# Kernel tuning notes

Measured on AMD Instinct MI355X. Metric: run time of the kernel, lower is better.

Reference implementation:

```python
import jax, jax.numpy as jnp
import numpy as np

DT = 1.0
V_LAMBDA = 1e-4
V_RIDGE = 1e-4


def third_order_D(Np):
    # [Np-3, Np] banded third-difference operator
    M = Np - 3
    r = jnp.arange(M)
    D = jnp.zeros((M, Np), dtype=jnp.float32)
    D = D.at[r, r].set(-1.0).at[r, r + 1].set(3.0).at[r, r + 2].set(-3.0).at[r, r + 3].set(1.0)
    return D


def setup_inputs() -> dict:
    key = jax.random.key(0)
    k1, k2, k3 = jax.random.split(key, 3)
    B, N = 8192, 64
    dxy = jax.random.normal(k1, (B, N, 2), dtype=jnp.float32)
    theta = jax.random.normal(k2, (B, N + 1), dtype=jnp.float32)
    v0 = jax.random.normal(k3, (B,), dtype=jnp.float32)
    return {"dxy": dxy, "theta": theta, "v0": v0}


def reference(dxy, theta, v0):
    B, N, _ = dxy.shape  # theta: [B, N+1]
    g = (2.0 / DT) * dxy                     # [B, N, 2]
    b = g.reshape(B, 2 * N)                  # interleaved (x, y) per step
    cos_t = jnp.cos(theta)
    sin_t = jnp.sin(theta)

    # Assemble banded data matrix A: [B, 2N, N+1]
    rows = jnp.arange(N)
    A = jnp.zeros((B, 2 * N, N + 1), dtype=dxy.dtype)
    A = A.at[:, 2 * rows, rows].set(cos_t[:, :-1])
    A = A.at[:, 2 * rows, rows + 1].set(cos_t[:, 1:])
    A = A.at[:, 2 * rows + 1, rows].set(sin_t[:, :-1])
    A = A.at[:, 2 * rows + 1, rows + 1].set(sin_t[:, 1:])
    # data weights w = 1 -> Aw == A

    ATA = jnp.einsum('bij,bik->bjk', A, A)           # [B, N+1, N+1]
    rhs = jnp.einsum('bij,bi->bj', A[:, :, 1:], b)   # [B, N]
    rhs = rhs - ATA[:, 1:, 0] * v0[:, None]

    # Smoothness prior: third-order difference, lam3 = v_lambda / dt^6
    D3 = third_order_D(N + 1)
    DTD = (V_LAMBDA / DT ** 6) * (D3.T @ D3)         # [N+1, N+1], shared across batch
    rhs = rhs - DTD[1:, 0] * v0[:, None]

    lhs = ATA[:, 1:, 1:] + DTD[1:, 1:] + V_RIDGE * jnp.eye(N, dtype=dxy.dtype)
    L = jnp.linalg.cholesky(lhs)
    y = jax.scipy.linalg.cho_solve((L, True), rhs[..., None])[..., 0]  # [B, N]
    return jnp.concatenate([v0[:, None], y], axis=-1)                  # [B, N+1]
```

## Files before the change

### kernel.cpp

```cpp
#include <hip/hip_runtime.h>
#include <math.h>

#define LAM3  1e-4f
#define RIDGE 1e-4f
#define NN    64
#define NP    65

__device__ __forceinline__ float d3_diag(int f) {
    if (f == 0 || f == 64) return 1.f;
    if (f == 1 || f == 63) return 10.f;
    if (f == 2 || f == 62) return 19.f;
    return 20.f;
}
__device__ __forceinline__ float d3_off1(int f) {
    if (f == 1 || f == 64) return -3.f;
    if (f == 2 || f == 63) return -12.f;
    return -15.f;
}
__device__ __forceinline__ float d3_off2(int f) {
    if (f == 2 || f == 64) return 3.f;
    return 6.f;
}

__global__ __launch_bounds__(64) void alpamayo_banded_solve(
    const float* __restrict__ dxy,
    const float* __restrict__ theta,
    const float* __restrict__ v0,
    float* __restrict__ out,
    int B)
{
    __shared__ float4 Lrec[NN][64];

    const int tid = threadIdx.x;
    const int b = blockIdx.x * 64 + tid;
    if (b >= B) return;

    const float* th = theta + (long)b * NP;
    const float* dx = dxy   + (long)b * (2 * NN);
    const float v0b = v0[b];

    float z[NN];

    float sp, cp;
    __sincosf(th[0], &sp, &cp);
    float bxp = 2.f * dx[0];
    float byp = 2.f * dx[1];

    float p1L1 = 0.f, p1L2 = 0.f, p2L1 = 0.f;
    float rd1 = 0.f, rd2 = 0.f, rd3 = 0.f;
    float z1 = 0.f, z2 = 0.f, z3 = 0.f;

    #pragma unroll
    for (int i = 0; i < NN; ++i) {
        const int f = i + 1;
        float sf, cf;
        __sincosf(th[f], &sf, &cf);
        const float e = cp * cf + sp * sf;

        float bxc = 0.f, byc = 0.f;
        if (f < NN) { bxc = 2.f * dx[2 * f]; byc = 2.f * dx[2 * f + 1]; }
        float rhs = cf * (bxp + bxc) + sf * (byp + byc);

        if (i == 0) rhs -= (e + LAM3 * -3.f) * v0b;
        if (i == 1) rhs -= (LAM3 *  3.f) * v0b;
        if (i == 2) rhs -= (LAM3 * -1.f) * v0b;

        const float a0 = (f == NN ? 1.f : 2.f) + LAM3 * d3_diag(f) + RIDGE;
        const float a1 = e + LAM3 * d3_off1(f);
        const float a2 = LAM3 * d3_off2(f);
        const float a3 = LAM3 * -1.f;

        const float Li3 = a3 * rd3;
        const float Li2 = (a2 - Li3 * p2L1) * rd2;
        const float Li1 = (a1 - Li3 * p1L2 - Li2 * p1L1) * rd1;
        const float dg  = a0 - Li3 * Li3 - Li2 * Li2 - Li1 * Li1;
        const float d   = sqrtf(dg);
        const float rd0 = 1.f / d;

        const float zi = (rhs - Li3 * z3 - Li2 * z2 - Li1 * z1) * rd0;

        Lrec[i][tid] = make_float4(Li1, Li2, Li3, rd0);
        z[i] = zi;

        p2L1 = p1L1; p1L1 = Li1; p1L2 = Li2;
        rd3 = rd2; rd2 = rd1; rd1 = rd0;
        z3 = z2; z2 = z1; z1 = zi;
        cp = cf; sp = sf; bxp = bxc; byp = byc;
    }

    float r1L1 = 0.f, r1L2 = 0.f, r1L3 = 0.f;
    float r2L2 = 0.f, r2L3 = 0.f;
    float r3L3 = 0.f;
    float y1 = 0.f, y2 = 0.f, y3 = 0.f;

    float* outp = out + (long)b * NP;

    #pragma unroll
    for (int i = NN - 1; i >= 0; --i) {
        const float4 rec = Lrec[i][tid];
        const float yi = (z[i] - r1L1 * y1 - r2L2 * y2 - r3L3 * y3) * rec.w;
        outp[1 + i] = yi;
        r3L3 = r2L3; r2L3 = r1L3; r2L2 = r1L2;
        r1L1 = rec.x; r1L2 = rec.y; r1L3 = rec.z;
        y3 = y2; y2 = y1; y1 = yi;
    }
    outp[0] = v0b;
}

extern "C" void kernel_launch(void* const* d_in, const int* in_sizes, int n_in,
                              void* d_out, int out_size, void* d_ws, size_t ws_size,
                              hipStream_t stream) {
    const float* dxy   = (const float*)d_in[0];
    const float* theta = (const float*)d_in[1];
    const float* v0    = (const float*)d_in[2];
    float* out = (float*)d_out;
    const int B = in_sizes[2];
    const int blocks = (B + 63) / 64;
    alpamayo_banded_solve<<<blocks, 64, 0, stream>>>(dxy, theta, v0, out, B);
}
```

Measured before the change: 68.45 us.

## Preload inputs into registers with vector loads and use hardware rsqrt

Loads all theta and dxy values for a row into registers up front, with float4 loads for dxy, and precomputes sin/cos, rhs and off-diagonal terms before the serial Cholesky recurrence. Replaces sqrt plus reciprocal with the AMDGCN rsq builtin and sets launch bounds to one block minimum. This is meant to take global-load latency and transcendental work off the dependent factorization chain and to issue more memory operations at once. It raises register pressure considerably, with possible spills, and lowers the precision of the reciprocal square root.

```diff
diff --git a/kernel.cpp b/kernel.cpp
--- a/kernel.cpp
+++ b/kernel.cpp
@@ -22,7 +22,7 @@
     return 6.f;
 }
 
-__global__ __launch_bounds__(64) void alpamayo_banded_solve(
+__global__ __launch_bounds__(64, 1) void alpamayo_banded_solve(
     const float* __restrict__ dxy,
     const float* __restrict__ theta,
     const float* __restrict__ v0,
@@ -36,16 +36,38 @@
     if (b >= B) return;
 
     const float* th = theta + (long)b * NP;
-    const float* dx = dxy   + (long)b * (2 * NN);
+    const float4* dx4 = (const float4*)(dxy + (long)b * (2 * NN));
     const float v0b = v0[b];
 
+    float thr[NP];
+    #pragma unroll
+    for (int f = 0; f < NP; ++f) thr[f] = th[f];
+    float dxf[2 * NN];
+    #pragma unroll
+    for (int j = 0; j < 32; ++j) {
+        const float4 q = dx4[j];
+        dxf[4 * j + 0] = q.x; dxf[4 * j + 1] = q.y;
+        dxf[4 * j + 2] = q.z; dxf[4 * j + 3] = q.w;
+    }
+
+    float c[NP], s[NP];
+    #pragma unroll
+    for (int f = 0; f < NP; ++f) __sincosf(thr[f], &s[f], &c[f]);
+
+    float rhs[NN], e[NN];
+    #pragma unroll
+    for (int i = 0; i < NN; ++i) {
+        const int f = i + 1;
+        const float bx = dxf[2 * f - 2] + (f < NN ? dxf[2 * f] : 0.f);
+        const float by = dxf[2 * f - 1] + (f < NN ? dxf[2 * f + 1] : 0.f);
+        rhs[i] = 2.f * (c[f] * bx + s[f] * by);
+        e[i] = c[i] * c[f] + s[i] * s[f];
+    }
+    rhs[0] -= (e[0] + LAM3 * -3.f) * v0b;
+    rhs[1] -= (LAM3 *  3.f) * v0b;
+    rhs[2] -= (LAM3 * -1.f) * v0b;
+
     float z[NN];
-
-    float sp, cp;
-    __sincosf(th[0], &sp, &cp);
-    float bxp = 2.f * dx[0];
-    float byp = 2.f * dx[1];
-
     float p1L1 = 0.f, p1L2 = 0.f, p2L1 = 0.f;
     float rd1 = 0.f, rd2 = 0.f, rd3 = 0.f;
     float z1 = 0.f, z2 = 0.f, z3 = 0.f;
@@ -53,20 +75,8 @@
     #pragma unroll
     for (int i = 0; i < NN; ++i) {
         const int f = i + 1;
-        float sf, cf;
-        __sincosf(th[f], &sf, &cf);
-        const float e = cp * cf + sp * sf;
-
-        float bxc = 0.f, byc = 0.f;
-        if (f < NN) { bxc = 2.f * dx[2 * f]; byc = 2.f * dx[2 * f + 1]; }
-        float rhs = cf * (bxp + bxc) + sf * (byp + byc);
-
-        if (i == 0) rhs -= (e + LAM3 * -3.f) * v0b;
-        if (i == 1) rhs -= (LAM3 *  3.f) * v0b;
-        if (i == 2) rhs -= (LAM3 * -1.f) * v0b;
-
         const float a0 = (f == NN ? 1.f : 2.f) + LAM3 * d3_diag(f) + RIDGE;
-        const float a1 = e + LAM3 * d3_off1(f);
+        const float a1 = e[i] + LAM3 * d3_off1(f);
         const float a2 = LAM3 * d3_off2(f);
         const float a3 = LAM3 * -1.f;
 
@@ -74,10 +84,9 @@
         const float Li2 = (a2 - Li3 * p2L1) * rd2;
         const float Li1 = (a1 - Li3 * p1L2 - Li2 * p1L1) * rd1;
         const float dg  = a0 - Li3 * Li3 - Li2 * Li2 - Li1 * Li1;
-        const float d   = sqrtf(dg);
-        const float rd0 = 1.f / d;
+        const float rd0 = __builtin_amdgcn_rsqf(dg);
 
-        const float zi = (rhs - Li3 * z3 - Li2 * z2 - Li1 * z1) * rd0;
+        const float zi = (rhs[i] - Li3 * z3 - Li2 * z2 - Li1 * z1) * rd0;
 
         Lrec[i][tid] = make_float4(Li1, Li2, Li3, rd0);
         z[i] = zi;
@@ -85,7 +94,6 @@
         p2L1 = p1L1; p1L1 = Li1; p1L2 = Li2;
         rd3 = rd2; rd2 = rd1; rd1 = rd0;
         z3 = z2; z2 = z1; z1 = zi;
-        cp = cf; sp = sf; bxp = bxc; byp = byc;
     }
 
     float r1L1 = 0.f, r1L2 = 0.f, r1L3 = 0.f;
```

Result: faster. 64.47 us (-5.8%).

## Stage inputs and outputs through shared memory with coalesced float4 transfers

Applied to the files above, without the earlier changes.

Each block now cooperatively loads its 64 rows of theta and dxy into shared memory with coalesced float4 reads and writes results back through shared memory with coalesced float4 stores. Previously each thread strided through its own row in global memory. The Cholesky factors are kept in register arrays instead of a shared float4 buffer, and the reciprocal square root uses the hardware rsq intrinsic. This raises shared memory and register use per block, which can lower occupancy, and the tail-handling guards on the float4 copies may drop a partial trailing vector when B is not a multiple of 64.

```diff
diff --git a/kernel.cpp b/kernel.cpp
--- a/kernel.cpp
+++ b/kernel.cpp
@@ -22,89 +22,124 @@
     return 6.f;
 }
 
-__global__ __launch_bounds__(64) void alpamayo_banded_solve(
+__global__ __launch_bounds__(64, 1) void alpamayo_banded_solve(
     const float* __restrict__ dxy,
     const float* __restrict__ theta,
     const float* __restrict__ v0,
     float* __restrict__ out,
     int B)
 {
-    __shared__ float4 Lrec[NN][64];
+    __shared__ float thS[64 * NP];
+    __shared__ float dxS[64 * 130];
 
     const int tid = threadIdx.x;
-    const int b = blockIdx.x * 64 + tid;
-    if (b >= B) return;
+    const long b0 = (long)blockIdx.x * 64;
+    const int b = (int)b0 + tid;
 
-    const float* th = theta + (long)b * NP;
-    const float* dx = dxy   + (long)b * (2 * NN);
-    const float v0b = v0[b];
+    {
+        const float4* g = (const float4*)(theta + b0 * NP);
+        float4* s4 = (float4*)thS;
+        const long lim = (long)B * NP - b0 * NP;
+        #pragma unroll
+        for (int it = 0; it < 17; ++it) {
+            const int k = it * 64 + tid;
+            if (k < 1040 && 4 * k + 3 < lim) s4[k] = g[k];
+        }
+    }
+    {
+        const float4* g = (const float4*)(dxy + b0 * 2 * NN);
+        const long lim4 = ((long)B * 2 * NN - b0 * 2 * NN) / 4;
+        #pragma unroll
+        for (int it = 0; it < 32; ++it) {
+            const int k = it * 64 + tid;
+            if (k < lim4) {
+                const float4 q = g[k];
+                const int flat = 4 * k;
+                const int addr = flat + 2 * (flat >> 7);
+                dxS[addr + 0] = q.x; dxS[addr + 1] = q.y;
+                dxS[addr + 2] = q.z; dxS[addr + 3] = q.w;
+            }
+        }
+    }
+    const float v0b = (b < B) ? v0[b] : 0.f;
+    __syncthreads();
 
-    float z[NN];
+    if (b < B) {
+        const float* thL = thS + tid * NP;
+        const float* dxL = dxS + tid * 130;
 
-    float sp, cp;
-    __sincosf(th[0], &sp, &cp);
-    float bxp = 2.f * dx[0];
-    float byp = 2.f * dx[1];
+        float L1a[NN], L2a[NN], L3a[NN], rda[NN], z[NN];
 
-    float p1L1 = 0.f, p1L2 = 0.f, p2L1 = 0.f;
-    float rd1 = 0.f, rd2 = 0.f, rd3 = 0.f;
-    float z1 = 0.f, z2 = 0.f, z3 = 0.f;
+        float sp, cp;
+        __sincosf(thL[0], &sp, &cp);
+        float bxp = dxL[0], byp = dxL[1];
 
-    #pragma unroll
-    for (int i = 0; i < NN; ++i) {
-        const int f = i + 1;
-        float sf, cf;
-        __sincosf(th[f], &sf, &cf);
-        const float e = cp * cf + sp * sf;
+        float p1L1 = 0.f, p1L2 = 0.f, p2L1 = 0.f;
+        float rd1 = 0.f, rd2 = 0.f, rd3 = 0.f;
+        float z1 = 0.f, z2 = 0.f, z3 = 0.f;
 
-        float bxc = 0.f, byc = 0.f;
-        if (f < NN) { bxc = 2.f * dx[2 * f]; byc = 2.f * dx[2 * f + 1]; }
-        float rhs = cf * (bxp + bxc) + sf * (byp + byc);
+        #pragma unroll
+        for (int i = 0; i < NN; ++i) {
+            const int f = i + 1;
+            float sf, cf;
+            __sincosf(thL[f], &sf, &cf);
+            const float e = cp * cf + sp * sf;
 
-        if (i == 0) rhs -= (e + LAM3 * -3.f) * v0b;
-        if (i == 1) rhs -= (LAM3 *  3.f) * v0b;
-        if (i == 2) rhs -= (LAM3 * -1.f) * v0b;
+            float bxc = 0.f, byc = 0.f;
+            if (f < NN) { bxc = dxL[2 * f]; byc = dxL[2 * f + 1]; }
+            float rhs = 2.f * (cf * (bxp + bxc) + sf * (byp + byc));
 
-        const float a0 = (f == NN ? 1.f : 2.f) + LAM3 * d3_diag(f) + RIDGE;
-        const float a1 = e + LAM3 * d3_off1(f);
-        const float a2 = LAM3 * d3_off2(f);
-        const float a3 = LAM3 * -1.f;
+            if (i == 0) rhs -= (e + LAM3 * -3.f) * v0b;
+            if (i == 1) rhs -= (LAM3 *  3.f) * v0b;
+            if (i == 2) rhs -= (LAM3 * -1.f) * v0b;
 
-        const float Li3 = a3 * rd3;
-        const float Li2 = (a2 - Li3 * p2L1) * rd2;
-        const float Li1 = (a1 - Li3 * p1L2 - Li2 * p1L1) * rd1;
-        const float dg  = a0 - Li3 * Li3 - Li2 * Li2 - Li1 * Li1;
-        const float d   = sqrtf(dg);
-        const float rd0 = 1.f / d;
+            const float a0 = (f == NN ? 1.f : 2.f) + LAM3 * d3_diag(f) + RIDGE;
+            const float a1 = e + LAM3 * d3_off1(f);
+            const float a2 = LAM3 * d3_off2(f);
+            const float a3 = LAM3 * -1.f;
 
-        const float zi = (rhs - Li3 * z3 - Li2 * z2 - Li1 * z1) * rd0;
+            const float Li3 = a3 * rd3;
+            const float Li2 = (a2 - Li3 * p2L1) * rd2;
+            const float Li1 = (a1 - Li3 * p1L2 - Li2 * p1L1) * rd1;
+            const float dg  = a0 - Li3 * Li3 - Li2 * Li2 - Li1 * Li1;
+            const float rd0 = __builtin_amdgcn_rsqf(dg);
 
-        Lrec[i][tid] = make_float4(Li1, Li2, Li3, rd0);
-        z[i] = zi;
+            const float zi = (rhs - Li3 * z3 - Li2 * z2 - Li1 * z1) * rd0;
 
-        p2L1 = p1L1; p1L1 = Li1; p1L2 = Li2;
-        rd3 = rd2; rd2 = rd1; rd1 = rd0;
-        z3 = z2; z2 = z1; z1 = zi;
-        cp = cf; sp = sf; bxp = bxc; byp = byc;
+            L1a[i] = Li1; L2a[i] = Li2; L3a[i] = Li3; rda[i] = rd0; z[i] = zi;
+
+            p2L1 = p1L1; p1L1 = Li1; p1L2 = Li2;
+            rd3 = rd2; rd2 = rd1; rd1 = rd0;
+            z3 = z2; z2 = z1; z1 = zi;
+            cp = cf; sp = sf; bxp = bxc; byp = byc;
+        }
+
+        float* yL = thS + tid * NP;
+        float y1 = 0.f, y2 = 0.f, y3 = 0.f;
+        #pragma unroll
+        for (int i = NN - 1; i >= 0; --i) {
+            float yi = z[i];
+            if (i + 1 < NN) yi -= L1a[i + 1] * y1;
+            if (i + 2 < NN) yi -= L2a[i + 2] * y2;
+            if (i + 3 < NN) yi -= L3a[i + 3] * y3;
+            yi *= rda[i];
+            yL[1 + i] = yi;
+            y3 = y2; y2 = y1; y1 = yi;
+        }
+        yL[0] = v0b;
     }
+    __syncthreads();
 
-    float r1L1 = 0.f, r1L2 = 0.f, r1L3 = 0.f;
-    float r2L2 = 0.f, r2L3 = 0.f;
-    float r3L3 = 0.f;
-    float y1 = 0.f, y2 = 0.f, y3 = 0.f;
-
-    float* outp = out + (long)b * NP;
-
-    #pragma unroll
-    for (int i = NN - 1; i >= 0; --i) {
-        const float4 rec = Lrec[i][tid];
-        const float yi = (z[i] - r1L1 * y1 - r2L2 * y2 - r3L3 * y3) * rec.w;
-        outp[1 + i] = yi;
-        r3L3 = r2L3; r2L3 = r1L3; r2L2 = r1L2;
-        r1L1 = rec.x; r1L2 = rec.y; r1L3 = rec.z;
-        y3 = y2; y2 = y1; y1 = yi;
+    {
+        float4* g = (float4*)(out + b0 * NP);
+        const float4* s4 = (const float4*)thS;
+        const long lim = (long)B * NP - b0 * NP;
+        #pragma unroll
+        for (int it = 0; it < 17; ++it) {
+            const int k = it * 64 + tid;
+            if (k < 1040 && 4 * k + 3 < lim) g[k] = s4[k];
+        }
     }
-    outp[0] = v0b;
 }
 
 extern "C" void kernel_launch(void* const* d_in, const int* in_sizes, int n_in,
```

Result: slower. 78.49 us (+14.7%).
